# Kernel optimization log

Hardware: AMD Instinct MI355X
Metric: run time of the kernel (lower is better)

The kernel has to match this reference:

```python
import math
import jax, jax.numpy as jnp
import numpy as np

B, CIN, COUT, K, S = 2, 64, 64, 3, 18  # batch, channels, kernel size per dim, spatial size per dim


def setup_inputs() -> dict:
    key = jax.random.key(0)
    k1, k2 = jax.random.split(key)
    inputs = jax.random.normal(k1, (B, CIN, S, S, S, S), dtype=jnp.float32)
    std = 1.0 / math.sqrt(CIN * K ** 4)  # matches init_weight: 1/sqrt(in_channels * n_offsets)
    kernel = jax.random.uniform(k2, (K ** 4, CIN, COUT), dtype=jnp.float32, minval=-std, maxval=std)
    return {"inputs": inputs, "kernel": kernel}


def reference(inputs, kernel):
    # kernel: [k0*k1*k2*k3, Cin, Cout], offsets enumerated row-major over the 4 kernel dims.
    # Equivalent to the per-offset matmul + shift-accumulate in conv4d (valid padding,
    # stride=1, dilation=1), expressed as a single 4-spatial-dim XLA convolution.
    cin, cout = kernel.shape[1], kernel.shape[2]
    w = kernel.reshape(K, K, K, K, cin, cout).transpose(5, 4, 0, 1, 2, 3)  # OIWXYZ
    out = jax.lax.conv_general_dilated(
        inputs, w,
        window_strides=(1, 1, 1, 1),
        padding='VALID',
        rhs_dilation=(1, 1, 1, 1),
        dimension_numbers=('NCWXYZ', 'OIWXYZ', 'NCWXYZ'),
    )  # [B, Cout, 16, 16, 16, 16]
    return out
```

## Files before the change

kernel.cpp:

```cpp
#include <hip/hip_runtime.h>


typedef __attribute__((ext_vector_type(8))) short bf16x8;
typedef __attribute__((ext_vector_type(4))) float f32x4;
typedef __attribute__((ext_vector_type(8))) unsigned short ushort8;
typedef unsigned short u16;
typedef unsigned int u32;

#define S_OFF_BYTES 663552u
#define WS_NEEDED   27537408u

__device__ __forceinline__ u16 f2bf(float f) {
    u32 u = __float_as_uint(f);
    u += 0x7FFFu + ((u >> 16) & 1u);
    return (u16)(u >> 16);
}

__global__ __launch_bounds__(256) void prep(const float* __restrict__ in,
                                            const float* __restrict__ ker,
                                            u16* __restrict__ s, u16* __restrict__ wg) {
    const int blk = blockIdx.x;
    const int t = threadIdx.x;
    if (blk >= 648) {
        const int g = (blk - 648) * 256 + t;
        const int l = g & 63, ks = (g >> 6) & 1, rt = (g >> 7) & 3, off = g >> 9;
        const int co  = rt * 16 + (l & 15);
        const int ci0 = ks * 32 + (l >> 4) * 8;
        const float* p = ker + (size_t)off * 4096 + co;
        ushort8 v;
#pragma unroll
        for (int e = 0; e < 8; ++e) v[e] = f2bf(p[(size_t)(ci0 + e) * 64]);
        *(ushort8*)(wg + (size_t)g * 8) = v;
        return;
    }
    __shared__ u16 L[64 * 330];
    const int b = blk / 324, wx = blk - b * 324;
    const float* src = in + (size_t)b * 6718464 + (wx / 18) * 5832 + (wx % 18) * 324;
    for (int i = t; i < 5184; i += 256) {
        const int ci = i / 81, j = i - ci * 81;
        float4 v = *(const float4*)(src + (size_t)ci * 104976 + j * 4);
        u32* q = (u32*)&L[ci * 330 + j * 4];
        q[0] = f2bf(v.x) | ((u32)f2bf(v.y) << 16);
        q[1] = f2bf(v.z) | ((u32)f2bf(v.w) << 16);
    }
    __syncthreads();
    u16* dst = s + (size_t)blk * 20736;
    for (int i = t; i < 2592; i += 256) {
        const int ks = i / 1296, r4 = i - ks * 1296;
        const int rem = r4 >> 2, g = r4 & 3;
        ushort8 v;
#pragma unroll
        for (int e = 0; e < 8; ++e) v[e] = L[(ks * 32 + g * 8 + e) * 330 + rem];
        const int gp = g ^ ((rem >> 1) & 3);
        *(ushort8*)(dst + ks * 10368 + rem * 32 + gp * 8) = v;
    }
}

__global__ __launch_bounds__(256, 1)
void conv4d_main(const u16* __restrict__ wg, const u16* __restrict__ s, float* __restrict__ out) {
    __shared__ u16 Bq[3][10368];

    const int bid = blockIdx.x;
    const int bs  = (bid & 7) * 64 + (bid >> 3);
    const int b   = bs >> 8;
    const int w   = (bs >> 4) & 15;
    const int x   = bs & 15;

    const int t  = threadIdx.x, wv = t >> 6, l = t & 63;
    const int lg = l >> 4, ll = l & 15;
    const int ch = wv >> 1;
    const int sh = wv & 1;

    f32x4 acc[2][8];
#pragma unroll
    for (int i = 0; i < 2; ++i)
#pragma unroll
        for (int j = 0; j < 8; ++j) acc[i][j] = (f32x4){0.f, 0.f, 0.f, 0.f};

    const u16* sb = s + (size_t)(b * 324 + w * 18 + x) * 20736;

    bf16x8 af[2][6];
    bf16x8 bb[2][10];

#define LOAD_A(BK, U)                                                                    \
    do {                                                                                 \
        const int tk_ = (U) / 3, kz_ = (U) % 3;                                          \
        const int kwx_ = tk_ >> 1, ks_ = tk_ & 1;                                        \
        _Pragma("unroll")                                                                \
        for (int ky_ = 0; ky_ < 3; ++ky_)                                                \
            _Pragma("unroll")                                                            \
            for (int rt_ = 0; rt_ < 2; ++rt_)                                            \
                af[BK][ky_ * 2 + rt_] = *(const bf16x8*)(wg                              \
                    + (size_t)(kwx_ * 9 + ky_ * 3 + kz_) * 4096                          \
                    + (size_t)(2 * ch + rt_) * 1024 + ks_ * 512 + l * 8);                \
    } while (0)

#define STAGE_B(h)                                                                       \
    do {                                                                                 \
        const int kwx_ = (h) >> 1, ks_ = (h) & 1;                                        \
        const int kw_ = kwx_ / 3, kx_ = kwx_ - kw_ * 3;                                  \
        const u16* src_ = sb + (size_t)(kw_ * 18 + kx_) * 20736 + ks_ * 10368;           \
        u16* dst_ = &Bq[(h) % 3][0];                                                     \
        const int base_ = wv * 324;                                                      \
        _Pragma("unroll")                                                                \
        for (int k_ = 0; k_ < 5; ++k_) {                                                 \
            const int i_ = base_ + k_ * 64 + l;                                          \
            __builtin_amdgcn_global_load_lds(                                            \
                (const __attribute__((address_space(1))) u32*)(src_ + (size_t)i_ * 8),   \
                (__attribute__((address_space(3))) u32*)(dst_ + i_ * 8), 16, 0, 0);      \
        }                                                                                \
        if (l < 4) {                                                                     \
            const int i_ = base_ + 320 + l;                                              \
            __builtin_amdgcn_global_load_lds(                                            \
                (const __attribute__((address_space(1))) u32*)(src_ + (size_t)i_ * 8),   \
                (__attribute__((address_space(3))) u32*)(dst_ + i_ * 8), 16, 0, 0);      \
        }                                                                                \
    } while (0)

#define READ_B(BK, SLOT3, KZ)                                                            \
    do {                                                                                 \
        const u16* Tb_ = &Bq[SLOT3][0];                                                  \
        _Pragma("unroll")                                                                \
        for (int j_ = 0; j_ < 10; ++j_) {                                                \
            const int rem_ = (8 * sh + j_) * 18 + ll + (KZ);                             \
            bb[BK][j_] = *(const bf16x8*)&Tb_[rem_ * 32 + ((lg ^ ((rem_ >> 1) & 3)) << 3)]; \
        }                                                                                \
    } while (0)

#define MFMA48(BK)                                                                       \
    do {                                                                                 \
        __builtin_amdgcn_s_setprio(1);                                                   \
        _Pragma("unroll")                                                                \
        for (int ky_ = 0; ky_ < 3; ++ky_)                                                \
            _Pragma("unroll")                                                            \
            for (int ct_ = 0; ct_ < 8; ++ct_)                                            \
                _Pragma("unroll")                                                        \
                for (int rt_ = 0; rt_ < 2; ++rt_)                                        \
                    acc[rt_][ct_] = __builtin_amdgcn_mfma_f32_16x16x32_bf16(             \
                        af[BK][ky_ * 2 + rt_], bb[BK][ct_ + ky_], acc[rt_][ct_], 0, 0, 0); \
        __builtin_amdgcn_s_setprio(0);                                                   \
    } while (0)

    STAGE_B(0);
    STAGE_B(1);
    LOAD_A(0, 0);
    asm volatile("s_waitcnt vmcnt(0)" ::: "memory");
    __builtin_amdgcn_sched_barrier(0);
    __builtin_amdgcn_s_barrier();
    READ_B(0, 0, 0);

    for (int u6 = 0; u6 < 54; u6 += 6) {
#pragma unroll
        for (int m = 0; m < 6; ++m) {
            const int u = u6 + m;
            const int p = u / 3;
            const int q = m % 3;
            const int cur = m & 1, nxt = cur ^ 1;
            if (u + 1 < 54) LOAD_A(nxt, u + 1);
            if (q == 0 && p + 2 < 18) STAGE_B(p + 2);
            if (q < 2)               READ_B(nxt, p % 3, q + 1);
            else if (p + 1 < 18)     READ_B(nxt, (p + 1) % 3, 0);
            __builtin_amdgcn_sched_barrier(0);
            MFMA48(cur);
            if (q == 2 && p < 17) {
                asm volatile("s_waitcnt vmcnt(12)" ::: "memory");
                __builtin_amdgcn_sched_barrier(0);
                __builtin_amdgcn_s_barrier();
            }
        }
    }
#undef LOAD_A
#undef STAGE_B
#undef READ_B
#undef MFMA48

    float* ob = out + (size_t)b * 4194304 + (size_t)w * 4096 + (size_t)x * 256;
#pragma unroll
    for (int rt = 0; rt < 2; ++rt) {
        const int co0 = ch * 32 + rt * 16 + 4 * lg;
#pragma unroll
        for (int ct = 0; ct < 8; ++ct) {
            const int base = (8 * sh + ct) * 16 + ll;
#pragma unroll
            for (int r = 0; r < 4; ++r)
                ob[(size_t)(co0 + r) * 65536 + base] = acc[rt][ct][r];
        }
    }
}

__global__ __launch_bounds__(512, 2)
void conv4d_mfma(const float* __restrict__ in, const float* __restrict__ ker,
                 float* __restrict__ out) {
    __shared__ unsigned short T[18 * 18 * 64];
    __shared__ unsigned short Wt[2][64 * 64];
    const int bx = blockIdx.x;
    const int b = bx >> 8, wsp = (bx >> 4) & 15, x = bx & 15;
    const int t = threadIdx.x, wv = t >> 6, l = t & 63;
    const int lg = l >> 4, ll = l & 15;
    const float* inb = in + (size_t)b * 6718464 + wsp * 5832 + x * 324;
    f32x4 acc[4][2];
#pragma unroll
    for (int i = 0; i < 4; ++i)
#pragma unroll
        for (int j = 0; j < 2; ++j) acc[i][j] = (f32x4){0.f, 0.f, 0.f, 0.f};
#pragma unroll
    for (int f0 = 0; f0 < 4096; f0 += 512) {
        const int f = f0 + t, ci = f >> 6, co = f & 63;
        Wt[0][co * 64 + ((((ci >> 3) ^ (co & 7)) << 3) | (ci & 7))] = f2bf(ker[f]);
    }
    for (int off = 0; off < 81; ++off) {
        const int sub = off % 9;
        if (sub == 0) {
            const int kw = off / 27, kx = (off / 9) % 3;
            const float* p = inb + kw * 5832 + kx * 324;
            for (int f = t; f < 18 * 18 * 64; f += 512) {
                const int ci = f / 324, rem = f - ci * 324, zp = rem % 18;
                T[rem * 64 + ((((ci >> 3) ^ (zp & 7)) << 3) | (ci & 7))] =
                    f2bf(p[(size_t)ci * 104976 + rem]);
            }
        }
        if (off + 1 < 81) {
            const float* p = ker + (off + 1) * 4096;
            unsigned short* wb = Wt[(off + 1) & 1];
#pragma unroll
            for (int f0 = 0; f0 < 4096; f0 += 512) {
                const int f = f0 + t, ci = f >> 6, co = f & 63;
                wb[co * 64 + ((((ci >> 3) ^ (co & 7)) << 3) | (ci & 7))] = f2bf(p[f]);
            }
        }
        if (sub == 0) __syncthreads();
        const int ky = sub / 3, kz = sub - ky * 3;
        const int zp = ll + kz, zs = zp & 7;
#pragma unroll
        for (int ks = 0; ks < 2; ++ks) {
            bf16x8 af[4];
#pragma unroll
            for (int rt = 0; rt < 4; ++rt)
                af[rt] = *(const bf16x8*)&Wt[off & 1][(rt * 16 + ll) * 64 + (((lg + 4 * ks) ^ (ll & 7)) << 3)];
#pragma unroll
            for (int ct = 0; ct < 2; ++ct) {
                const int rem = (2 * wv + ct + ky) * 18 + zp;
                const bf16x8 bfr = *(const bf16x8*)&T[rem * 64 + (((lg + 4 * ks) ^ zs) << 3)];
#pragma unroll
                for (int rt = 0; rt < 4; ++rt)
                    acc[rt][ct] = __builtin_amdgcn_mfma_f32_16x16x32_bf16(af[rt], bfr, acc[rt][ct], 0, 0, 0);
            }
        }
        __syncthreads();
    }
    float* ob = out + (size_t)b * 4194304 + wsp * 4096 + x * 256;
#pragma unroll
    for (int rt = 0; rt < 4; ++rt) {
        const int co0 = rt * 16 + 4 * lg;
#pragma unroll
        for (int ct = 0; ct < 2; ++ct) {
            const int base = (2 * wv + ct) * 16 + ll;
#pragma unroll
            for (int r = 0; r < 4; ++r)
                ob[(size_t)(co0 + r) * 65536 + base] = acc[rt][ct][r];
        }
    }
}

extern "C" void kernel_launch(void* const* d_in, const int* in_sizes, int n_in,
                              void* d_out, int out_size, void* d_ws, size_t ws_size,
                              hipStream_t stream) {
    const float* in  = (const float*)d_in[0];
    const float* ker = (const float*)d_in[1];
    float* out = (float*)d_out;
    if (ws_size >= (size_t)WS_NEEDED) {
        u16* wg = (u16*)d_ws;
        u16* s  = (u16*)((char*)d_ws + S_OFF_BYTES);
        prep<<<dim3(810), dim3(256), 0, stream>>>(in, ker, s, wg);
        conv4d_main<<<dim3(512), dim3(256), 0, stream>>>(wg, s, out);
    } else {
        conv4d_mfma<<<dim3(512), dim3(512), 0, stream>>>(in, ker, out);
    }
}
```

Measured before the change: 101.0 us.

## Read input fragments directly from global memory instead of LDS staging

Removes the triple-buffered shared-memory staging of input tiles (global_load_lds plus barriers) and has each wave load its B fragments straight from global memory into registers. Barriers and explicit waitcnt and sched_barrier pipelining go away, leaving the compiler to schedule loads around the MFMAs. The risk is more global/L2 traffic, since waves sharing data each fetch it again, and exposed global latency before the MFMAs.

```diff
diff --git a/kernel.cpp b/kernel.cpp
--- a/kernel.cpp
+++ b/kernel.cpp
@@ -58,8 +58,6 @@
 
 __global__ __launch_bounds__(256, 1)
 void conv4d_main(const u16* __restrict__ wg, const u16* __restrict__ s, float* __restrict__ out) {
-    __shared__ u16 Bq[3][10368];
-
     const int bid = blockIdx.x;
     const int bs  = (bid & 7) * 64 + (bid >> 3);
     const int b   = bs >> 8;
@@ -95,34 +93,15 @@
                     + (size_t)(2 * ch + rt_) * 1024 + ks_ * 512 + l * 8);                \
     } while (0)
 
-#define STAGE_B(h)                                                                       \
+#define READ_B(BK, U)                                                                    \
     do {                                                                                 \
-        const int kwx_ = (h) >> 1, ks_ = (h) & 1;                                        \
+        const int tk_ = (U) / 3, kz_ = (U) % 3;                                          \
+        const int kwx_ = tk_ >> 1, ks_ = tk_ & 1;                                        \
         const int kw_ = kwx_ / 3, kx_ = kwx_ - kw_ * 3;                                  \
-        const u16* src_ = sb + (size_t)(kw_ * 18 + kx_) * 20736 + ks_ * 10368;           \
-        u16* dst_ = &Bq[(h) % 3][0];                                                     \
-        const int base_ = wv * 324;                                                      \
-        _Pragma("unroll")                                                                \
-        for (int k_ = 0; k_ < 5; ++k_) {                                                 \
-            const int i_ = base_ + k_ * 64 + l;                                          \
-            __builtin_amdgcn_global_load_lds(                                            \
-                (const __attribute__((address_space(1))) u32*)(src_ + (size_t)i_ * 8),   \
-                (__attribute__((address_space(3))) u32*)(dst_ + i_ * 8), 16, 0, 0);      \
-        }                                                                                \
-        if (l < 4) {                                                                     \
-            const int i_ = base_ + 320 + l;                                              \
-            __builtin_amdgcn_global_load_lds(                                            \
-                (const __attribute__((address_space(1))) u32*)(src_ + (size_t)i_ * 8),   \
-                (__attribute__((address_space(3))) u32*)(dst_ + i_ * 8), 16, 0, 0);      \
-        }                                                                                \
-    } while (0)
-
-#define READ_B(BK, SLOT3, KZ)                                                            \
-    do {                                                                                 \
-        const u16* Tb_ = &Bq[SLOT3][0];                                                  \
+        const u16* Tb_ = sb + (size_t)(kw_ * 18 + kx_) * 20736 + ks_ * 10368;            \
         _Pragma("unroll")                                                                \
         for (int j_ = 0; j_ < 10; ++j_) {                                                \
-            const int rem_ = (8 * sh + j_) * 18 + ll + (KZ);                             \
+            const int rem_ = (8 * sh + j_) * 18 + ll + kz_;                              \
             bb[BK][j_] = *(const bf16x8*)&Tb_[rem_ * 32 + ((lg ^ ((rem_ >> 1) & 3)) << 3)]; \
         }                                                                                \
     } while (0)
@@ -141,36 +120,22 @@
         __builtin_amdgcn_s_setprio(0);                                                   \
     } while (0)
 
-    STAGE_B(0);
-    STAGE_B(1);
     LOAD_A(0, 0);
-    asm volatile("s_waitcnt vmcnt(0)" ::: "memory");
-    __builtin_amdgcn_sched_barrier(0);
-    __builtin_amdgcn_s_barrier();
-    READ_B(0, 0, 0);
+    READ_B(0, 0);
 
     for (int u6 = 0; u6 < 54; u6 += 6) {
 #pragma unroll
         for (int m = 0; m < 6; ++m) {
             const int u = u6 + m;
-            const int p = u / 3;
-            const int q = m % 3;
             const int cur = m & 1, nxt = cur ^ 1;
-            if (u + 1 < 54) LOAD_A(nxt, u + 1);
-            if (q == 0 && p + 2 < 18) STAGE_B(p + 2);
-            if (q < 2)               READ_B(nxt, p % 3, q + 1);
-            else if (p + 1 < 18)     READ_B(nxt, (p + 1) % 3, 0);
-            __builtin_amdgcn_sched_barrier(0);
+            if (u + 1 < 54) {
+                LOAD_A(nxt, u + 1);
+                READ_B(nxt, u + 1);
+            }
             MFMA48(cur);
-            if (q == 2 && p < 17) {
-                asm volatile("s_waitcnt vmcnt(12)" ::: "memory");
-                __builtin_amdgcn_sched_barrier(0);
-                __builtin_amdgcn_s_barrier();
-            }
         }
     }
 #undef LOAD_A
-#undef STAGE_B
 #undef READ_B
 #undef MFMA48
 
```

Result: faster. 91.20 us (-9.7%).
